# Optimization experiments

Hardware: AMD Instinct MI355X
Metric: run time of the kernel (lower is better)

## Reference

```python
import jax, jax.numpy as jnp
import numpy as np

IN_F = 4096
OUT_F = 4096

def setup_inputs() -> dict:
    key = jax.random.key(0)
    k1, k2 = jax.random.split(key)
    x = jax.random.normal(k1, (8, 2048, IN_F), dtype=jnp.float32)
    weight = jax.random.normal(k2, (OUT_F, IN_F), dtype=jnp.float32) * 0.1
    bias = jnp.zeros((OUT_F,), dtype=jnp.float32)
    return {"x": x, "weight": weight, "bias": bias}

def reference(x, weight, bias):
    # binarize weights to +-1 with per-row abs-mean scale
    binary_w = jnp.sign(weight)
    scale = jnp.mean(jnp.abs(weight), axis=1, keepdims=True)  # [OUT_F, 1]
    w = scale * binary_w
    # F.linear: x @ w.T + bias
    return jnp.einsum('bsi,oi->bso', x, w) + bias
```

## Files before the change

### kernel.cpp

```cpp
#include <hip/hip_runtime.h>
#include <hip/hip_bf16.h>

#define M_TOT 16384
#define N_TOT 4096
#define K_TOT 4096

typedef __attribute__((ext_vector_type(8))) short bf16x8;
typedef __attribute__((ext_vector_type(4))) float f32x4;

typedef const __attribute__((address_space(1))) void* gptr_t;
typedef __attribute__((address_space(3))) void* lptr_t;

__device__ inline unsigned short f2bf(float f) {
    union { float f; unsigned u; } v; v.f = f;
    unsigned u = v.u;
    u += 0x7FFFu + ((u >> 16) & 1u);
    return (unsigned short)(u >> 16);
}

__device__ inline unsigned short sgn_bf(float f) {
    union { float f; unsigned u; } v; v.f = f;
    return (unsigned short)(((v.u >> 16) & 0x8000u) | 0x3F80u);
}

__global__ void prep_weight(const float* __restrict__ w,
                            unsigned short* __restrict__ bw,
                            float* __restrict__ scale) {
    const int row = blockIdx.x;
    const int tid = threadIdx.x;
    const float4* wr = (const float4*)(w + (size_t)row * K_TOT);
    float s = 0.f;
#pragma unroll
    for (int i = 0; i < 4; ++i) {
        int idx = tid + i * 256;
        float4 v = wr[idx];
        s += fabsf(v.x) + fabsf(v.y) + fabsf(v.z) + fabsf(v.w);
        if (bw) {
            ushort4 b;
            b.x = sgn_bf(v.x); b.y = sgn_bf(v.y);
            b.z = sgn_bf(v.z); b.w = sgn_bf(v.w);
            *(ushort4*)(bw + (size_t)row * K_TOT + idx * 4) = b;
        }
    }
#pragma unroll
    for (int off = 32; off > 0; off >>= 1) s += __shfl_down(s, off, 64);
    __shared__ float red[4];
    if ((tid & 63) == 0) red[tid >> 6] = s;
    __syncthreads();
    if (tid == 0) scale[row] = (red[0] + red[1] + red[2] + red[3]) * (1.f / (float)K_TOT);
}

__global__ void conv_x(const float* __restrict__ x, unsigned short* __restrict__ xb) {
    const long n4 = (long)M_TOT * K_TOT / 4;
    long i = (long)blockIdx.x * blockDim.x + threadIdx.x;
    const long stride = (long)gridDim.x * blockDim.x;
    for (; i < n4; i += stride) {
        float4 v = ((const float4*)x)[i];
        ushort4 b;
        b.x = f2bf(v.x); b.y = f2bf(v.y); b.z = f2bf(v.z); b.w = f2bf(v.w);
        ((ushort4*)xb)[i] = b;
    }
}

__global__ __launch_bounds__(256) void gemm_bin_dma(const unsigned short* __restrict__ A,
                                                    const unsigned short* __restrict__ B,
                                                    const float* __restrict__ scale,
                                                    const float* __restrict__ bias,
                                                    float* __restrict__ out) {
    __shared__ unsigned short As[128 * 32];
    __shared__ unsigned short Bs[128 * 32];

    const int tid  = threadIdx.x;
    const int wave = tid >> 6;
    const int lane = tid & 63;
    const int quad = lane >> 4;
    const int l16  = lane & 15;
    const int wr   = wave >> 1;
    const int wc   = wave & 1;
    const int bn   = blockIdx.x * 128;
    const int bm   = blockIdx.y * 128;

    const int srow = lane >> 2;
    const int scol = (lane & 3) * 8;

    f32x4 acc[4][4] = {};

    for (int kt = 0; kt < K_TOT; kt += 32) {
#pragma unroll
        for (int p = 0; p < 2; ++p) {
            const int rowbase = wave * 32 + p * 16;
            const unsigned short* ga =
                A + (size_t)(bm + rowbase + srow) * K_TOT + kt + scol;
            __builtin_amdgcn_global_load_lds((gptr_t)ga, (lptr_t)(As + rowbase * 32),
                                             16, 0, 0);
            const unsigned short* gb =
                B + (size_t)(bn + rowbase + srow) * K_TOT + kt + scol;
            __builtin_amdgcn_global_load_lds((gptr_t)gb, (lptr_t)(Bs + rowbase * 32),
                                             16, 0, 0);
        }
        __syncthreads();

        bf16x8 af[4], bfr[4];
#pragma unroll
        for (int i = 0; i < 4; ++i)
            af[i] = *(const bf16x8*)&As[(wr * 64 + i * 16 + l16) * 32 + quad * 8];
#pragma unroll
        for (int j = 0; j < 4; ++j)
            bfr[j] = *(const bf16x8*)&Bs[(wc * 64 + j * 16 + l16) * 32 + quad * 8];
#pragma unroll
        for (int i = 0; i < 4; ++i)
#pragma unroll
            for (int j = 0; j < 4; ++j)
                acc[i][j] = __builtin_amdgcn_mfma_f32_16x16x32_bf16(af[i], bfr[j], acc[i][j], 0, 0, 0);
        __syncthreads();
    }

#pragma unroll
    for (int j = 0; j < 4; ++j) {
        const int gn = bn + wc * 64 + j * 16 + l16;
        const float sc = scale[gn];
        const float bi = bias[gn];
#pragma unroll
        for (int i = 0; i < 4; ++i) {
            const int gm0 = bm + wr * 64 + i * 16 + quad * 4;
#pragma unroll
            for (int r = 0; r < 4; ++r)
                out[(size_t)(gm0 + r) * N_TOT + gn] = acc[i][j][r] * sc + bi;
        }
    }
}

__global__ __launch_bounds__(256) void gemm_bin_fb(const float* __restrict__ A,
                                                   const float* __restrict__ Bf,
                                                   const float* __restrict__ scale,
                                                   const float* __restrict__ bias,
                                                   float* __restrict__ out) {
    __shared__ unsigned short As[128][40];
    __shared__ unsigned short Bs[128][40];

    const int tid  = threadIdx.x;
    const int wave = tid >> 6;
    const int lane = tid & 63;
    const int quad = lane >> 4;
    const int l16  = lane & 15;
    const int wr   = wave >> 1;
    const int wc   = wave & 1;
    const int bn   = blockIdx.x * 128;
    const int bm   = blockIdx.y * 128;

    f32x4 acc[4][4] = {};

    for (int kt = 0; kt < K_TOT; kt += 32) {
        const int row0 = tid >> 3;
        const int c4   = (tid & 7) * 4;
#pragma unroll
        for (int p = 0; p < 4; ++p) {
            int row = row0 + p * 32;
            float4 v = *(const float4*)(A + (size_t)(bm + row) * K_TOT + kt + c4);
            ushort4 b;
            b.x = f2bf(v.x); b.y = f2bf(v.y); b.z = f2bf(v.z); b.w = f2bf(v.w);
            *(ushort4*)&As[row][c4] = b;
        }
#pragma unroll
        for (int p = 0; p < 4; ++p) {
            int row = row0 + p * 32;
            float4 v = *(const float4*)(Bf + (size_t)(bn + row) * K_TOT + kt + c4);
            ushort4 b;
            b.x = sgn_bf(v.x); b.y = sgn_bf(v.y); b.z = sgn_bf(v.z); b.w = sgn_bf(v.w);
            *(ushort4*)&Bs[row][c4] = b;
        }
        __syncthreads();

        bf16x8 af[4], bfr[4];
#pragma unroll
        for (int i = 0; i < 4; ++i)
            af[i] = *(const bf16x8*)&As[wr * 64 + i * 16 + l16][quad * 8];
#pragma unroll
        for (int j = 0; j < 4; ++j)
            bfr[j] = *(const bf16x8*)&Bs[wc * 64 + j * 16 + l16][quad * 8];
#pragma unroll
        for (int i = 0; i < 4; ++i)
#pragma unroll
            for (int j = 0; j < 4; ++j)
                acc[i][j] = __builtin_amdgcn_mfma_f32_16x16x32_bf16(af[i], bfr[j], acc[i][j], 0, 0, 0);
        __syncthreads();
    }

#pragma unroll
    for (int j = 0; j < 4; ++j) {
        const int gn = bn + wc * 64 + j * 16 + l16;
        const float sc = scale[gn];
        const float bi = bias[gn];
#pragma unroll
        for (int i = 0; i < 4; ++i) {
            const int gm0 = bm + wr * 64 + i * 16 + quad * 4;
#pragma unroll
            for (int r = 0; r < 4; ++r)
                out[(size_t)(gm0 + r) * N_TOT + gn] = acc[i][j][r] * sc + bi;
        }
    }
}

extern "C" void kernel_launch(void* const* d_in, const int* in_sizes, int n_in,
                              void* d_out, int out_size, void* d_ws, size_t ws_size,
                              hipStream_t stream) {
    const float* x    = (const float*)d_in[0];
    const float* w    = (const float*)d_in[1];
    const float* bias = (const float*)d_in[2];
    float* out        = (float*)d_out;

    const size_t off_scale = 0;
    const size_t off_bw    = 16384;
    const size_t off_xb    = off_bw + (size_t)N_TOT * K_TOT * 2;
    const size_t need_full = off_xb + (size_t)M_TOT * K_TOT * 2;

    float* scale = (float*)((char*)d_ws + off_scale);
    const bool full = ws_size >= need_full;

    dim3 grid(N_TOT / 128, M_TOT / 128);

    if (full) {
        unsigned short* bw = (unsigned short*)((char*)d_ws + off_bw);
        unsigned short* xb = (unsigned short*)((char*)d_ws + off_xb);
        prep_weight<<<N_TOT, 256, 0, stream>>>(w, bw, scale);
        conv_x<<<8192, 256, 0, stream>>>(x, xb);
        gemm_bin_dma<<<grid, 256, 0, stream>>>(xb, bw, scale, bias, out);
    } else {
        prep_weight<<<N_TOT, 256, 0, stream>>>(w, nullptr, scale);
        gemm_bin_fb<<<grid, 256, 0, stream>>>(x, w, scale, bias, out);
    }
}
```

Measured before the change: 1.098 ms.

## Replace bf16 GEMM with 256x256-tile, 8-wave, double-buffered 8-phase pipelined kernel

Replaces the 128x128-tile, single-buffered GEMM, which waits on a barrier every 32-wide K step, with a 256x256-tile kernel using 512 threads. It double-buffers 64-wide K slices in LDS through direct global-to-LDS loads, interleaves the loads with MFMA phases, and uses vmcnt waits and s_setprio. It also XOR-swizzles the LDS layout to avoid bank conflicts and remaps block IDs for better L2 locality. The aim is to hide memory latency and raise data reuse per tile, at the cost of heavy register pressure (128 accumulator floats per thread) and hand-tuned waitcnt logic that is fragile.

```diff
diff --git a/kernel.cpp b/kernel.cpp
--- a/kernel.cpp
+++ b/kernel.cpp
@@ -62,13 +62,171 @@
     }
 }
 
-__global__ __launch_bounds__(256) void gemm_bin_dma(const unsigned short* __restrict__ A,
-                                                    const unsigned short* __restrict__ B,
-                                                    const float* __restrict__ scale,
-                                                    const float* __restrict__ bias,
-                                                    float* __restrict__ out) {
-    __shared__ unsigned short As[128 * 32];
-    __shared__ unsigned short Bs[128 * 32];
+#define AS0 0
+#define BS0 16384
+#define AS1 32768
+#define BS1 49152
+
+#define STAGE(Mat, row0, ldsbase, h, ktv)                                         \
+  {                                                                               \
+    _Pragma("unroll")                                                             \
+    for (int c_ = 0; c_ < 2; ++c_) {                                              \
+      const unsigned short* g_ = (Mat) +                                          \
+          (size_t)((row0) + (h)*128 + c_*64 + wv*8 + srow) * K_TOT + (ktv) + scol;\
+      __builtin_amdgcn_global_load_lds((gptr_t)g_,                                \
+          (lptr_t)(lds + (ldsbase) + ((h)*128 + c_*64 + wv*8) * 64), 16, 0, 0);   \
+    }                                                                             \
+  }
+
+#define DS_A(h, base)                                                             \
+  {                                                                               \
+    _Pragma("unroll")                                                             \
+    for (int i_ = 0; i_ < 4; ++i_) {                                              \
+      _Pragma("unroll")                                                           \
+      for (int k_ = 0; k_ < 2; ++k_) {                                            \
+        int off_ = (wr*128 + (h)*64 + i_*16 + l16)*128 + k_*64 + quad*16;         \
+        off_ ^= ((off_ >> 9) & 1) << 5;                                           \
+        af[i_][k_] = *(const bf16x8*)((const char*)(lds + (base)) + off_);        \
+      }                                                                           \
+    }                                                                             \
+  }
+
+#define DS_B(dst, g, base)                                                        \
+  {                                                                               \
+    _Pragma("unroll")                                                             \
+    for (int j_ = 0; j_ < 2; ++j_) {                                              \
+      _Pragma("unroll")                                                           \
+      for (int k_ = 0; k_ < 2; ++k_) {                                            \
+        int ob_ = (wc*64 + (g)*32 + j_*16 + l16)*128 + k_*64 + quad*16;           \
+        ob_ ^= ((ob_ >> 9) & 1) << 5;                                             \
+        dst[j_][k_] = *(const bf16x8*)((const char*)(lds + (base)) + ob_);        \
+      }                                                                           \
+    }                                                                             \
+  }
+
+#define MMA(h, g, bset)                                                           \
+  {                                                                               \
+    __builtin_amdgcn_s_setprio(1);                                                \
+    _Pragma("unroll")                                                             \
+    for (int i_ = 0; i_ < 4; ++i_) {                                              \
+      _Pragma("unroll")                                                           \
+      for (int j_ = 0; j_ < 2; ++j_) {                                            \
+        acc[(h)*4+i_][(g)*2+j_] = __builtin_amdgcn_mfma_f32_16x16x32_bf16(        \
+            af[i_][0], bset[j_][0], acc[(h)*4+i_][(g)*2+j_], 0, 0, 0);            \
+        acc[(h)*4+i_][(g)*2+j_] = __builtin_amdgcn_mfma_f32_16x16x32_bf16(        \
+            af[i_][1], bset[j_][1], acc[(h)*4+i_][(g)*2+j_], 0, 0, 0);            \
+      }                                                                           \
+    }                                                                             \
+    __builtin_amdgcn_s_setprio(0);                                                \
+  }
+
+#define BAR1  { __builtin_amdgcn_s_barrier(); asm volatile("s_waitcnt lgkmcnt(0)"); }
+#define BAR2  { __builtin_amdgcn_s_barrier(); }
+#define VM4   { asm volatile("s_waitcnt vmcnt(4)" ::: "memory"); }
+#define VM0   { asm volatile("s_waitcnt vmcnt(0)" ::: "memory"); }
+
+__global__ __launch_bounds__(512, 2) void gemm_bin_8ph(
+    const unsigned short* __restrict__ A,
+    const unsigned short* __restrict__ B,
+    const float* __restrict__ scale,
+    const float* __restrict__ bias,
+    float* __restrict__ out) {
+    __shared__ unsigned short lds[4 * 16384];
+
+    const int tid  = threadIdx.x;
+    const int wv   = tid >> 6;
+    const int lane = tid & 63;
+    const int quad = lane >> 4;
+    const int l16  = lane & 15;
+    const int wr   = wv >> 2;
+    const int wc   = wv & 3;
+
+    int bid = blockIdx.x;
+    bid = (bid & 7) * 128 + (bid >> 3);
+    const int bn = (bid & 15) * 256;
+    const int bm = (bid >> 4) * 256;
+
+    const int srow = lane >> 3;
+    const int scol = ((lane & 7) * 8) ^ (((lane >> 5) & 1) << 4);
+
+    f32x4 acc[8][4] = {};
+    bf16x8 af[4][2], bl[2][2], bh[2][2];
+
+    STAGE(A, bm, AS0, 0, 0)
+    STAGE(A, bm, AS0, 1, 0)
+    STAGE(B, bn, BS0, 0, 0)
+    STAGE(B, bn, BS0, 1, 0)
+    STAGE(B, bn, BS1, 0, 64)
+    STAGE(B, bn, BS1, 1, 64)
+    asm volatile("s_waitcnt vmcnt(4)" ::: "memory");
+    __builtin_amdgcn_s_barrier();
+
+    int kt = 0;
+#pragma unroll 1
+    for (int t = 0; t < (K_TOT / 128) - 1; ++t, kt += 128) {
+        DS_A(0, AS0) DS_B(bl, 0, BS0)
+        STAGE(A, bm, AS1, 0, kt + 64)
+        BAR1 MMA(0, 0, bl) BAR2
+        DS_B(bh, 1, BS0)
+        STAGE(A, bm, AS1, 1, kt + 64)
+        BAR1 MMA(0, 1, bh) BAR2
+        DS_A(1, AS0)
+        STAGE(B, bn, BS0, 0, kt + 128)
+        BAR1 MMA(1, 1, bh) BAR2
+        STAGE(B, bn, BS0, 1, kt + 128)
+        BAR1 MMA(1, 0, bl) VM4 BAR2
+        DS_A(0, AS1) DS_B(bl, 0, BS1)
+        STAGE(A, bm, AS0, 0, kt + 128)
+        BAR1 MMA(0, 0, bl) BAR2
+        DS_B(bh, 1, BS1)
+        STAGE(A, bm, AS0, 1, kt + 128)
+        BAR1 MMA(0, 1, bh) BAR2
+        DS_A(1, AS1)
+        STAGE(B, bn, BS1, 0, kt + 192)
+        BAR1 MMA(1, 1, bh) BAR2
+        STAGE(B, bn, BS1, 1, kt + 192)
+        BAR1 MMA(1, 0, bl) VM4 BAR2
+    }
+
+    DS_A(0, AS0) DS_B(bl, 0, BS0)
+    STAGE(A, bm, AS1, 0, kt + 64)
+    BAR1 MMA(0, 0, bl) BAR2
+    DS_B(bh, 1, BS0)
+    STAGE(A, bm, AS1, 1, kt + 64)
+    BAR1 MMA(0, 1, bh) BAR2
+    DS_A(1, AS0)
+    BAR1 MMA(1, 1, bh) BAR2
+    BAR1 MMA(1, 0, bl) VM0 BAR2
+    DS_A(0, AS1) DS_B(bl, 0, BS1)
+    BAR1 MMA(0, 0, bl) BAR2
+    DS_B(bh, 1, BS1)
+    BAR1 MMA(0, 1, bh) BAR2
+    DS_A(1, AS1)
+    BAR1 MMA(1, 1, bh) BAR2
+    BAR1 MMA(1, 0, bl)
+
+#pragma unroll
+    for (int j4 = 0; j4 < 4; ++j4) {
+        const int gn = bn + wc * 64 + j4 * 16 + l16;
+        const float sc = scale[gn];
+        const float bi = bias[gn];
+#pragma unroll
+        for (int i8 = 0; i8 < 8; ++i8) {
+            const int gm0 = bm + wr * 128 + i8 * 16 + quad * 4;
+#pragma unroll
+            for (int r = 0; r < 4; ++r)
+                out[(size_t)(gm0 + r) * N_TOT + gn] = acc[i8][j4][r] * sc + bi;
+        }
+    }
+}
+
+__global__ __launch_bounds__(256) void gemm_bin_fb(const float* __restrict__ A,
+                                                   const float* __restrict__ Bf,
+                                                   const float* __restrict__ scale,
+                                                   const float* __restrict__ bias,
+                                                   float* __restrict__ out) {
+    __shared__ unsigned short As[128][40];
+    __shared__ unsigned short Bs[128][40];
 
     const int tid  = threadIdx.x;
     const int wave = tid >> 6;
@@ -80,74 +238,6 @@
     const int bn   = blockIdx.x * 128;
     const int bm   = blockIdx.y * 128;
 
-    const int srow = lane >> 2;
-    const int scol = (lane & 3) * 8;
-
-    f32x4 acc[4][4] = {};
-
-    for (int kt = 0; kt < K_TOT; kt += 32) {
-#pragma unroll
-        for (int p = 0; p < 2; ++p) {
-            const int rowbase = wave * 32 + p * 16;
-            const unsigned short* ga =
-                A + (size_t)(bm + rowbase + srow) * K_TOT + kt + scol;
-            __builtin_amdgcn_global_load_lds((gptr_t)ga, (lptr_t)(As + rowbase * 32),
-                                             16, 0, 0);
-            const unsigned short* gb =
-                B + (size_t)(bn + rowbase + srow) * K_TOT + kt + scol;
-            __builtin_amdgcn_global_load_lds((gptr_t)gb, (lptr_t)(Bs + rowbase * 32),
-                                             16, 0, 0);
-        }
-        __syncthreads();
-
-        bf16x8 af[4], bfr[4];
-#pragma unroll
-        for (int i = 0; i < 4; ++i)
-            af[i] = *(const bf16x8*)&As[(wr * 64 + i * 16 + l16) * 32 + quad * 8];
-#pragma unroll
-        for (int j = 0; j < 4; ++j)
-            bfr[j] = *(const bf16x8*)&Bs[(wc * 64 + j * 16 + l16) * 32 + quad * 8];
-#pragma unroll
-        for (int i = 0; i < 4; ++i)
-#pragma unroll
-            for (int j = 0; j < 4; ++j)
-                acc[i][j] = __builtin_amdgcn_mfma_f32_16x16x32_bf16(af[i], bfr[j], acc[i][j], 0, 0, 0);
-        __syncthreads();
-    }
-
-#pragma unroll
-    for (int j = 0; j < 4; ++j) {
-        const int gn = bn + wc * 64 + j * 16 + l16;
-        const float sc = scale[gn];
-        const float bi = bias[gn];
-#pragma unroll
-        for (int i = 0; i < 4; ++i) {
-            const int gm0 = bm + wr * 64 + i * 16 + quad * 4;
-#pragma unroll
-            for (int r = 0; r < 4; ++r)
-                out[(size_t)(gm0 + r) * N_TOT + gn] = acc[i][j][r] * sc + bi;
-        }
-    }
-}
-
-__global__ __launch_bounds__(256) void gemm_bin_fb(const float* __restrict__ A,
-                                                   const float* __restrict__ Bf,
-                                                   const float* __restrict__ scale,
-                                                   const float* __restrict__ bias,
-                                                   float* __restrict__ out) {
-    __shared__ unsigned short As[128][40];
-    __shared__ unsigned short Bs[128][40];
-
-    const int tid  = threadIdx.x;
-    const int wave = tid >> 6;
-    const int lane = tid & 63;
-    const int quad = lane >> 4;
-    const int l16  = lane & 15;
-    const int wr   = wave >> 1;
-    const int wc   = wave & 1;
-    const int bn   = blockIdx.x * 128;
-    const int bm   = blockIdx.y * 128;
-
     f32x4 acc[4][4] = {};
 
     for (int kt = 0; kt < K_TOT; kt += 32) {
@@ -171,10 +261,10 @@
         }
         __syncthreads();
 
-        bf16x8 af[4], bfr[4];
+        bf16x8 af2[4], bfr[4];
 #pragma unroll
         for (int i = 0; i < 4; ++i)
-            af[i] = *(const bf16x8*)&As[wr * 64 + i * 16 + l16][quad * 8];
+            af2[i] = *(const bf16x8*)&As[wr * 64 + i * 16 + l16][quad * 8];
 #pragma unroll
         for (int j = 0; j < 4; ++j)
             bfr[j] = *(const bf16x8*)&Bs[wc * 64 + j * 16 + l16][quad * 8];
@@ -182,7 +272,7 @@
         for (int i = 0; i < 4; ++i)
 #pragma unroll
             for (int j = 0; j < 4; ++j)
-                acc[i][j] = __builtin_amdgcn_mfma_f32_16x16x32_bf16(af[i], bfr[j], acc[i][j], 0, 0, 0);
+                acc[i][j] = __builtin_amdgcn_mfma_f32_16x16x32_bf16(af2[i], bfr[j], acc[i][j], 0, 0, 0);
         __syncthreads();
     }
 
@@ -217,16 +307,16 @@
     float* scale = (float*)((char*)d_ws + off_scale);
     const bool full = ws_size >= need_full;
 
-    dim3 grid(N_TOT / 128, M_TOT / 128);
-
     if (full) {
         unsigned short* bw = (unsigned short*)((char*)d_ws + off_bw);
         unsigned short* xb = (unsigned short*)((char*)d_ws + off_xb);
         prep_weight<<<N_TOT, 256, 0, stream>>>(w, bw, scale);
         conv_x<<<8192, 256, 0, stream>>>(x, xb);
-        gemm_bin_dma<<<grid, 256, 0, stream>>>(xb, bw, scale, bias, out);
+        const int nwg = (M_TOT / 256) * (N_TOT / 256);
+        gemm_bin_8ph<<<nwg, 512, 0, stream>>>(xb, bw, scale, bias, out);
     } else {
         prep_weight<<<N_TOT, 256, 0, stream>>>(w, nullptr, scale);
+        dim3 grid(N_TOT / 128, M_TOT / 128);
         gemm_bin_fb<<<grid, 256, 0, stream>>>(x, w, scale, bias, out);
     }
 }
```

Result: faster. 950.3 us (-13.5%).
